# Kernel optimization log

Measured on AMD Instinct MI355X. Metric: run time of the kernel, lower is better.

Reference implementation:

```python
import jax, jax.numpy as jnp
import numpy as np

B, Hh, Ww, C, HEADS, WS, SHIFT = 8, 64, 64, 768, 12, 8, 4
N = WS * WS
HID = 4 * C


def _rel_pos_index(ws):
    coords = np.stack(np.meshgrid(np.arange(ws), np.arange(ws), indexing='ij'))  # (2, ws, ws)
    cf = coords.reshape(2, -1)
    rel = (cf[:, :, None] - cf[:, None, :]).transpose(1, 2, 0)  # (N, N, 2)
    rel[:, :, 0] += ws - 1
    rel[:, :, 1] += ws - 1
    rel[:, :, 0] *= 2 * ws - 1
    return rel.sum(-1)  # (N, N) in [0, (2ws-1)^2)


def _attn_mask(Hp, Wp, ws, shift):
    # Standard Swin shifted-window attention mask: 0 within region, -100 across.
    img = np.zeros((Hp, Wp), dtype=np.float32)
    cnt = 0
    sls = (slice(0, -ws), slice(-ws, -shift), slice(-shift, None))
    for hs in sls:
        for wsl in sls:
            img[hs, wsl] = cnt
            cnt += 1
    w = img.reshape(Hp // ws, ws, Wp // ws, ws).transpose(0, 2, 1, 3).reshape(-1, ws * ws)
    diff = w[:, None, :] - w[:, :, None]
    return np.where(diff != 0, -100.0, 0.0).astype(np.float32)  # (nW, N, N)


def setup_inputs() -> dict:
    key = jax.random.key(0)
    ks = jax.random.split(key, 8)
    s = 0.02
    return {
        'x': jax.random.normal(ks[0], (B, Hh * Ww, C), jnp.float32),
        'c': jax.random.normal(ks[1], (B, C), jnp.float32),
        'mask_matrix': jnp.asarray(_attn_mask(Hh, Ww, WS, SHIFT)),
        'rel_index': jnp.asarray(_rel_pos_index(WS), dtype=jnp.int32),
        'w_adaln': jax.random.normal(ks[2], (C, 6 * C), jnp.float32) * s,
        'b_adaln': jnp.zeros((6 * C,), jnp.float32),
        'w_qkv': jax.random.normal(ks[3], (C, 3 * C), jnp.float32) * s,
        'b_qkv': jnp.zeros((3 * C,), jnp.float32),
        'rpb_table': jax.random.normal(ks[4], ((2 * WS - 1) ** 2, HEADS), jnp.float32) * s,
        'w_proj': jax.random.normal(ks[5], (C, C), jnp.float32) * s,
        'b_proj': jnp.zeros((C,), jnp.float32),
        'w_fc1': jax.random.normal(ks[6], (C, HID), jnp.float32) * s,
        'b_fc1': jnp.zeros((HID,), jnp.float32),
        'w_fc2': jax.random.normal(ks[7], (HID, C), jnp.float32) * s,
        'b_fc2': jnp.zeros((C,), jnp.float32),
        'H': Hh,
        'W': Ww,
    }


def _ln(x, eps=1e-6):
    # LayerNorm without affine params (elementwise_affine=False)
    mu = x.mean(-1, keepdims=True)
    var = x.var(-1, keepdims=True)
    return (x - mu) * jax.lax.rsqrt(var + eps)


def _modulate(x, shift, scale):
    return x * (1.0 + scale[:, None, :]) + shift[:, None, :]


def reference(x, c, mask_matrix, rel_index, w_adaln, b_adaln, w_qkv, b_qkv,
              rpb_table, w_proj, b_proj, w_fc1, b_fc1, w_fc2, b_fc2, H, W):
    Bb, L, Cc = x.shape
    hd = Cc // HEADS
    mod = jax.nn.silu(c) @ w_adaln + b_adaln  # (B, 6C)
    sh_msa, sc_msa, g_msa, sh_mlp, sc_mlp, g_mlp = jnp.split(mod, 6, axis=1)

    shortcut = x
    h = _modulate(_ln(x), sh_msa, sc_msa).reshape(Bb, H, W, Cc)
    # H,W are multiples of WS -> no padding; shift_size>0 -> roll + mask
    h = jnp.roll(h, (-SHIFT, -SHIFT), axis=(1, 2))
    nWh, nWw = H // WS, W // WS
    win = h.reshape(Bb, nWh, WS, nWw, WS, Cc).transpose(0, 1, 3, 2, 4, 5).reshape(-1, N, Cc)

    qkv = (win @ w_qkv + b_qkv).reshape(-1, N, 3, HEADS, hd).transpose(2, 0, 3, 1, 4)
    q = qkv[0] * (hd ** -0.5)
    k, v = qkv[1], qkv[2]
    attn = jnp.einsum('bhnd,bhmd->bhnm', q, k)  # (B_, heads, N, N)
    bias = rpb_table[rel_index.reshape(-1)].reshape(N, N, HEADS).transpose(2, 0, 1)
    attn = attn + bias[None]
    nW = mask_matrix.shape[0]
    attn = attn.reshape(Bb, nW, HEADS, N, N) + mask_matrix[None, :, None]
    attn = jax.nn.softmax(attn.reshape(-1, HEADS, N, N), axis=-1)
    out = jnp.einsum('bhnm,bhmd->bnhd', attn, v).reshape(-1, N, Cc)
    out = out @ w_proj + b_proj

    out = out.reshape(Bb, nWh, nWw, WS, WS, Cc).transpose(0, 1, 3, 2, 4, 5).reshape(Bb, H, W, Cc)
    out = jnp.roll(out, (SHIFT, SHIFT), axis=(1, 2)).reshape(Bb, L, Cc)

    x1 = shortcut + g_msa[:, None, :] * out
    h2 = _modulate(_ln(x1), sh_mlp, sc_mlp)
    mlp = jax.nn.gelu(h2 @ w_fc1 + b_fc1, approximate=False) @ w_fc2 + b_fc2
    return x1 + g_mlp[:, None, :] * mlp
```

## Files before the change

kernel.cpp:

```cpp
#include <hip/hip_runtime.h>
#include <hip/hip_bf16.h>
#include <math.h>

using bf16 = __hip_bfloat16;
using short8  = __attribute__((ext_vector_type(8))) short;
using floatx4 = __attribute__((ext_vector_type(4))) float;

__device__ __forceinline__ float b2f(bf16 v){ return __bfloat162float(v); }
__device__ __forceinline__ bf16  f2b(float v){ return __float2bfloat16(v); }
__device__ __forceinline__ float loadf(const void* p, size_t i, bool f32){
    return f32 ? ((const float*)p)[i] : b2f(((const bf16*)p)[i]);
}
__device__ __forceinline__ void gload16(const void* g, void* l){
    __builtin_amdgcn_global_load_lds(
        (const __attribute__((address_space(1))) unsigned int*)g,
        (__attribute__((address_space(3))) unsigned int*)l, 16, 0, 0);
}
__device__ __forceinline__ void bar(){
    asm volatile("" ::: "memory");
    __builtin_amdgcn_s_barrier();
    asm volatile("" ::: "memory");
}
template<int Nn> __device__ __forceinline__ void vmwait(){
    if constexpr (Nn == 0)      asm volatile("s_waitcnt vmcnt(0)" ::: "memory");
    else if constexpr (Nn == 3) asm volatile("s_waitcnt vmcnt(3)" ::: "memory");
    else                        asm volatile("s_waitcnt vmcnt(4)" ::: "memory");
}
__device__ __forceinline__ void lgkm0_fence(){
    asm volatile("s_waitcnt lgkmcnt(0)" ::: "memory");
    __builtin_amdgcn_sched_barrier(0);
}

#define FIXED_WS 14303488

__global__ void detect_k(const void* __restrict__ x, int* __restrict__ flag){
    __shared__ int cnt;
    if (threadIdx.x == 0) cnt = 0;
    __syncthreads();
    const unsigned short* u = (const unsigned short*)x;
    int local = 0;
    #pragma unroll
    for (int i = 0; i < 16; ++i){
        unsigned int w = u[threadIdx.x * 16 + i];
        float v = __uint_as_float(w << 16);
        float a = fabsf(v);
        if (!(a <= 1e4f) || (v != 0.f && a < 1e-20f)) local++;
    }
    atomicAdd(&cnt, local);
    __syncthreads();
    if (threadIdx.x == 0) *flag = (cnt > 200) ? 1 : 0;
}

__global__ void transpose_k(const void* __restrict__ W, bf16* __restrict__ WT, int K, int N,
                            const int* __restrict__ dflag){
    const bool f32 = (*dflag != 0);
    __shared__ bf16 t[32][33];
    int k0 = blockIdx.y * 32, n0 = blockIdx.x * 32;
    int tx = threadIdx.x, ty = threadIdx.y;
    #pragma unroll
    for (int r = ty; r < 32; r += 8) t[r][tx] = f2b(loadf(W, (size_t)(k0 + r) * N + n0 + tx, f32));
    __syncthreads();
    #pragma unroll
    for (int r = ty; r < 32; r += 8) WT[(size_t)(n0 + r) * K + k0 + tx] = t[tx][r];
}

__global__ __launch_bounds__(256) void adaln_k(const void* __restrict__ c, const void* __restrict__ w,
                                               const void* __restrict__ bv, float* __restrict__ mod,
                                               const int* __restrict__ dflag){
    const bool f32 = (*dflag != 0);
    int b = blockIdx.y;
    int jl = threadIdx.x & 63;
    int part = threadIdx.x >> 6;
    int j = blockIdx.x * 64 + jl;
    __shared__ float sc[768];
    for (int k = threadIdx.x; k < 768; k += 256){
        float v = loadf(c, b * 768 + k, f32);
        sc[k] = v / (1.f + __expf(-v));
    }
    __syncthreads();
    float acc = 0.f;
    int k0 = part * 192;
    #pragma unroll 4
    for (int k = k0; k < k0 + 192; ++k) acc += sc[k] * loadf(w, (size_t)k * 4608 + j, f32);
    __shared__ float red[4][64];
    red[part][jl] = acc;
    __syncthreads();
    if (part == 0)
        mod[b * 4608 + j] = red[0][jl] + red[1][jl] + red[2][jl] + red[3][jl] + loadf(bv, j, f32);
}

__device__ __forceinline__ float2 block_reduce_sum2(float s, float s2){
    #pragma unroll
    for (int m = 32; m >= 1; m >>= 1){
        s  += __shfl_xor(s,  m, 64);
        s2 += __shfl_xor(s2, m, 64);
    }
    __shared__ float red[8];
    int wave = threadIdx.x >> 6;
    if ((threadIdx.x & 63) == 0){ red[wave] = s; red[4 + wave] = s2; }
    __syncthreads();
    return make_float2(red[0] + red[1] + red[2] + red[3],
                       red[4] + red[5] + red[6] + red[7]);
}

__global__ __launch_bounds__(256) void ln_mod_win_k(const void* __restrict__ x, const float* __restrict__ mod,
                                                    bf16* __restrict__ win, int roff,
                                                    const int* __restrict__ dflag){
    const bool f32 = (*dflag != 0);
    int r = roff + blockIdx.x;
    int bw = r >> 6, n = r & 63;
    int b = bw >> 6, widx = bw & 63;
    int hh = (((widx >> 3) << 3) + (n >> 3) + 4) & 63;
    int ww = (((widx & 7) << 3) + (n & 7) + 4) & 63;
    size_t xo = ((size_t)b * 4096 + hh * 64 + ww) * 768;
    int t = threadIdx.x;
    float v0 = loadf(x, xo + t, f32), v1 = loadf(x, xo + t + 256, f32), v2 = loadf(x, xo + t + 512, f32);
    float2 ss = block_reduce_sum2(v0 + v1 + v2, v0 * v0 + v1 * v1 + v2 * v2);
    float mu = ss.x * (1.f / 768.f);
    float rstd = rsqrtf(ss.y * (1.f / 768.f) - mu * mu + 1e-6f);
    const float* mb = mod + b * 4608;
    bf16* wr = win + (size_t)blockIdx.x * 768;
    wr[t]       = f2b((v0 - mu) * rstd * (1.f + mb[768 + t])       + mb[t]);
    wr[t + 256] = f2b((v1 - mu) * rstd * (1.f + mb[768 + t + 256]) + mb[t + 256]);
    wr[t + 512] = f2b((v2 - mu) * rstd * (1.f + mb[768 + t + 512]) + mb[t + 512]);
}

__global__ __launch_bounds__(256) void ln_mod2_k(const void* __restrict__ x1, const float* __restrict__ mod,
                                                 bf16* __restrict__ h2, int roff,
                                                 const int* __restrict__ dflag){
    const bool f32 = (*dflag != 0);
    int t0 = roff + blockIdx.x;
    int b = t0 >> 12;
    size_t xo = (size_t)t0 * 768;
    int t = threadIdx.x;
    float v0 = loadf(x1, xo + t, f32), v1 = loadf(x1, xo + t + 256, f32), v2 = loadf(x1, xo + t + 512, f32);
    float2 ss = block_reduce_sum2(v0 + v1 + v2, v0 * v0 + v1 * v1 + v2 * v2);
    float mu = ss.x * (1.f / 768.f);
    float rstd = rsqrtf(ss.y * (1.f / 768.f) - mu * mu + 1e-6f);
    const float* mb = mod + b * 4608;
    bf16* wr = h2 + (size_t)blockIdx.x * 768;
    wr[t]       = f2b((v0 - mu) * rstd * (1.f + mb[3072 + t])       + mb[2304 + t]);
    wr[t + 256] = f2b((v1 - mu) * rstd * (1.f + mb[3072 + t + 256]) + mb[2304 + t + 256]);
    wr[t + 512] = f2b((v2 - mu) * rstd * (1.f + mb[3072 + t + 512]) + mb[2304 + t + 512]);
}

__global__ __launch_bounds__(256) void attn_k(const bf16* __restrict__ qkv, const void* __restrict__ maskm,
                                              const int* __restrict__ rel, const void* __restrict__ rpb,
                                              bf16* __restrict__ ao, int woff,
                                              const int* __restrict__ dflag){
    const bool f32 = (*dflag != 0);
    __shared__ bf16  qs[64][68];
    __shared__ float ks[64][65];
    __shared__ bf16  vs[64][64];
    __shared__ float Ps[64][68];
    int blk = blockIdx.x;
    int head = blk % 12;
    int bw = blk / 12;
    int tid = threadIdx.x;
    const bf16* base = qkv + (size_t)bw * 64 * 2304 + head * 64;
    for (int e4 = tid; e4 < 1024; e4 += 256){
        int n = e4 >> 4, d4 = (e4 & 15) * 4;
        size_t o = (size_t)n * 2304 + d4;
        ushort4 qv = *(const ushort4*)(base + o);
        ushort4 kv = *(const ushort4*)(base + o + 768);
        ushort4 vv = *(const ushort4*)(base + o + 1536);
        bf16 q0, q1, q2, q3;
        *(unsigned short*)&q0 = qv.x; *(unsigned short*)&q1 = qv.y;
        *(unsigned short*)&q2 = qv.z; *(unsigned short*)&q3 = qv.w;
        qs[n][d4]     = f2b(b2f(q0) * 0.125f);
        qs[n][d4 + 1] = f2b(b2f(q1) * 0.125f);
        qs[n][d4 + 2] = f2b(b2f(q2) * 0.125f);
        qs[n][d4 + 3] = f2b(b2f(q3) * 0.125f);
        bf16 k0, k1, k2, k3;
        *(unsigned short*)&k0 = kv.x; *(unsigned short*)&k1 = kv.y;
        *(unsigned short*)&k2 = kv.z; *(unsigned short*)&k3 = kv.w;
        ks[n][d4]     = b2f(k0); ks[n][d4 + 1] = b2f(k1);
        ks[n][d4 + 2] = b2f(k2); ks[n][d4 + 3] = b2f(k3);
        *(ushort4*)&vs[n][d4] = vv;
    }
    __syncthreads();
    size_t mo = (size_t)((woff + bw) & 63) * 4096;
    int i0 = (tid >> 4) * 4, j0 = (tid & 15) * 4;
    {
        float acc[4][4];
        #pragma unroll
        for (int a = 0; a < 4; ++a)
            #pragma unroll
            for (int b2 = 0; b2 < 4; ++b2) acc[a][b2] = 0.f;
        #pragma unroll 8
        for (int d = 0; d < 64; ++d){
            float qv[4], kv[4];
            #pragma unroll
            for (int a = 0; a < 4; ++a) qv[a] = b2f(qs[i0 + a][d]);
            #pragma unroll
            for (int b2 = 0; b2 < 4; ++b2) kv[b2] = ks[j0 + b2][d];
            #pragma unroll
            for (int a = 0; a < 4; ++a)
                #pragma unroll
                for (int b2 = 0; b2 < 4; ++b2) acc[a][b2] += qv[a] * kv[b2];
        }
        #pragma unroll
        for (int a = 0; a < 4; ++a){
            int i = i0 + a;
            int4 r4 = *(const int4*)&rel[i * 64 + j0];
            float4 o4;
            o4.x = acc[a][0] + loadf(rpb, (size_t)r4.x * 12 + head, f32) + loadf(maskm, mo + i * 64 + j0,     f32);
            o4.y = acc[a][1] + loadf(rpb, (size_t)r4.y * 12 + head, f32) + loadf(maskm, mo + i * 64 + j0 + 1, f32);
            o4.z = acc[a][2] + loadf(rpb, (size_t)r4.z * 12 + head, f32) + loadf(maskm, mo + i * 64 + j0 + 2, f32);
            o4.w = acc[a][3] + loadf(rpb, (size_t)r4.w * 12 + head, f32) + loadf(maskm, mo + i * 64 + j0 + 3, f32);
            *(float4*)&Ps[i][j0] = o4;
        }
    }
    __syncthreads();
    {
        int row = tid >> 2, p0 = (tid & 3) * 16;
        float mx = -1e30f;
        #pragma unroll
        for (int j = 0; j < 16; ++j) mx = fmaxf(mx, Ps[row][p0 + j]);
        mx = fmaxf(mx, __shfl_xor(mx, 1, 64));
        mx = fmaxf(mx, __shfl_xor(mx, 2, 64));
        float sum = 0.f;
        float ev[16];
        #pragma unroll
        for (int j = 0; j < 16; ++j){ ev[j] = __expf(Ps[row][p0 + j] - mx); sum += ev[j]; }
        sum += __shfl_xor(sum, 1, 64);
        sum += __shfl_xor(sum, 2, 64);
        float inv = 1.f / sum;
        #pragma unroll
        for (int j = 0; j < 16; ++j) Ps[row][p0 + j] = ev[j] * inv;
    }
    __syncthreads();
    {
        int d0 = j0;
        float po[4][4];
        #pragma unroll
        for (int a = 0; a < 4; ++a)
            #pragma unroll
            for (int b2 = 0; b2 < 4; ++b2) po[a][b2] = 0.f;
        #pragma unroll 8
        for (int j = 0; j < 64; ++j){
            float pv[4];
            #pragma unroll
            for (int a = 0; a < 4; ++a) pv[a] = Ps[i0 + a][j];
            ushort4 v4 = *(const ushort4*)&vs[j][d0];
            bf16 w0, w1, w2, w3;
            *(unsigned short*)&w0 = v4.x; *(unsigned short*)&w1 = v4.y;
            *(unsigned short*)&w2 = v4.z; *(unsigned short*)&w3 = v4.w;
            float vv[4] = {b2f(w0), b2f(w1), b2f(w2), b2f(w3)};
            #pragma unroll
            for (int a = 0; a < 4; ++a)
                #pragma unroll
                for (int b2 = 0; b2 < 4; ++b2) po[a][b2] += pv[a] * vv[b2];
        }
        #pragma unroll
        for (int a = 0; a < 4; ++a){
            ushort4 s4;
            bf16 t0 = f2b(po[a][0]), t1 = f2b(po[a][1]), t2 = f2b(po[a][2]), t3 = f2b(po[a][3]);
            s4.x = *(unsigned short*)&t0; s4.y = *(unsigned short*)&t1;
            s4.z = *(unsigned short*)&t2; s4.w = *(unsigned short*)&t3;
            *(ushort4*)&ao[((size_t)bw * 64 + i0 + a) * 768 + head * 64 + d0] = s4;
        }
    }
}

template<int EPI, int BN>
__global__ __launch_bounds__(256, (BN == 128) ? 3 : 4)
void gemm_k(const bf16* __restrict__ A, const bf16* __restrict__ BT,
            const void* __restrict__ bias, void* __restrict__ Cout,
            int N, int K, int roff,
            const void* __restrict__ xres, const float* __restrict__ mod,
            const void* __restrict__ x1,
            const int* __restrict__ dflag, int nMB){
    constexpr int MFR = (BN == 128) ? 4 : 2;
    constexpr int LPT = (BN == 128) ? 4 : 3;
    const bool f32 = (*dflag != 0);
    __shared__ __align__(16) bf16 As[3][128 * 32];
    __shared__ __align__(16) bf16 Bs[3][BN * 32];

    int bid = (int)blockIdx.x;
    int nb = bid / nMB, mb = bid % nMB;
    int m0 = mb * 128, n0 = nb * BN;

    int tid = threadIdx.x;
    int wave = tid >> 6, lane = tid & 63;
    int wm = (BN == 128) ? (wave >> 1) * 64 : wave * 32;
    int wn = (BN == 128) ? (wave & 1) * 64 : 0;
    int lrow = lane & 15, lq = lane >> 4;
    floatx4 acc[MFR][4];
    #pragma unroll
    for (int i = 0; i < MFR; ++i)
        #pragma unroll
        for (int j = 0; j < 4; ++j) acc[i][j] = floatx4{0.f, 0.f, 0.f, 0.f};

    int sc8 = ((((lane & 3) - ((lane >> 3) & 3)) & 3)) * 8;
    int srw = lane >> 2;
    const bf16* gA = A + (size_t)(m0 + wave * 32 + srw) * K + sc8;
    int lofsA0 = (wave * 32) * 32;
    int lofsA1 = (wave * 32 + 16) * 32;
    const bf16* gB;
    int lofsB;
    if constexpr (BN == 128){ gB = BT + (size_t)(n0 + wave * 32 + srw) * K + sc8; lofsB = lofsA0; }
    else                    { gB = BT + (size_t)(n0 + wave * 16 + srw) * K + sc8; lofsB = (wave * 16) * 32; }

    int fsw = ((lq + ((lrow >> 1) & 3)) & 3) * 8;
    int aoff = (wm + lrow) * 32 + fsw;
    int boff = (wn + lrow) * 32 + fsw;

    auto stage = [&](int t, int buf){
        size_t kof = (size_t)t * 32;
        gload16(gA + kof,                  As[buf] + lofsA0);
        gload16(gA + kof + (size_t)16 * K, As[buf] + lofsA1);
        gload16(gB + kof,                  Bs[buf] + lofsB);
        if constexpr (BN == 128)
            gload16(gB + kof + (size_t)16 * K, Bs[buf] + lofsA1);
    };

    const int nkt = K >> 5;
    stage(0, 0); stage(1, 1);
    vmwait<LPT>();
    bar();
    int cur = 0, nx2 = 2;
    for (int t = 0; t < nkt; ++t){
        short8 af[MFR], bfr[4];
        #pragma unroll
        for (int f = 0; f < MFR; ++f) af[f]  = *(const short8*)(As[cur] + aoff + f * 512);
        #pragma unroll
        for (int f = 0; f < 4;   ++f) bfr[f] = *(const short8*)(Bs[cur] + boff + f * 512);
        if (t + 2 < nkt) stage(t + 2, nx2);
        lgkm0_fence();
        __builtin_amdgcn_s_setprio(1);
        #pragma unroll
        for (int mf = 0; mf < MFR; ++mf)
            #pragma unroll
            for (int nf = 0; nf < 4; ++nf)
                acc[mf][nf] = __builtin_amdgcn_mfma_f32_16x16x32_bf16(af[mf], bfr[nf], acc[mf][nf], 0, 0, 0);
        __builtin_amdgcn_s_setprio(0);
        if (t + 2 < nkt) vmwait<LPT>();
        else             vmwait<0>();
        bar();
        cur = (cur == 2) ? 0 : cur + 1;
        nx2 = (nx2 == 2) ? 0 : nx2 + 1;
    }

    #pragma unroll
    for (int mf = 0; mf < MFR; ++mf){
        #pragma unroll
        for (int nf = 0; nf < 4; ++nf){
            #pragma unroll
            for (int rr = 0; rr < 4; ++rr){
                int grow = m0 + wm + mf * 16 + lq * 4 + rr;
                int gcol = n0 + wn + nf * 16 + lrow;
                float v = acc[mf][nf][rr] + loadf(bias, gcol, f32);
                if (EPI == 0){
                    ((bf16*)Cout)[(size_t)grow * N + gcol] = f2b(v);
                } else if (EPI == 1){
                    float g = 0.5f * v * (1.f + erff(v * 0.70710678118654752f));
                    ((bf16*)Cout)[(size_t)grow * N + gcol] = f2b(g);
                } else if (EPI == 2){
                    int gr = roff + grow;
                    int bw = gr >> 6, n = gr & 63;
                    int b = bw >> 6, widx = bw & 63;
                    int hh = (((widx >> 3) << 3) + (n >> 3) + 4) & 63;
                    int ww = (((widx & 7) << 3) + (n & 7) + 4) & 63;
                    size_t t = ((size_t)b * 4096 + hh * 64 + ww) * 768 + gcol;
                    float gm = mod[b * 4608 + 1536 + gcol];
                    float res = loadf(xres, t, f32) + gm * v;
                    if (f32) ((float*)Cout)[t] = res; else ((bf16*)Cout)[t] = f2b(res);
                } else {
                    int gr = roff + grow;
                    int b = gr >> 12;
                    float gm = mod[b * 4608 + 3840 + gcol];
                    size_t t = (size_t)gr * N + gcol;
                    float res = loadf(x1, t, f32) + gm * v;
                    if (f32) ((float*)Cout)[t] = res; else ((bf16*)Cout)[t] = f2b(res);
                }
            }
        }
    }
}

extern "C" void kernel_launch(void* const* d_in, const int* in_sizes, int n_in,
                              void* d_out, int out_size, void* d_ws, size_t ws_size,
                              hipStream_t stream){
    const void* x       = d_in[0];
    const void* c       = d_in[1];
    const void* maskm   = d_in[2];
    const int*  rel     = (const int*)d_in[3];
    const void* w_adaln = d_in[4];
    const void* b_adaln = d_in[5];
    const void* w_qkv   = d_in[6];
    const void* b_qkv   = d_in[7];
    const void* rpb     = d_in[8];
    const void* w_proj  = d_in[9];
    const void* b_proj  = d_in[10];
    const void* w_fc1   = d_in[11];
    const void* b_fc1   = d_in[12];
    const void* w_fc2   = d_in[13];
    const void* b_fc2   = d_in[14];

    int Mc = 4096;
    for (int cand = 8192; cand >= 256; cand >>= 1){
        if (FIXED_WS + (size_t)cand * 7680u <= ws_size){ Mc = cand; break; }
    }
    const int nc  = 32768 / Mc;
    const int nMB = Mc / 128;

    char* ws = (char*)d_ws;
    int*  dflag  = (int*)(ws);
    float* mod   = (float*)(ws + 256);
    bf16* wqkvT  = (bf16*)(ws + 147712);
    bf16* wprojT = (bf16*)(ws + 3686656);
    bf16* wfc1T  = (bf16*)(ws + 4866304);
    bf16* wfc2T  = (bf16*)(ws + 9584896);
    bf16* win_c  = (bf16*)(ws + FIXED_WS);
    bf16* big_c  = (bf16*)(ws + FIXED_WS + (size_t)Mc * 1536);
    bf16* ao_c   = (bf16*)(ws + FIXED_WS + (size_t)Mc * 6144);
    void* x1     = d_out;
    void* out    = d_out;

    detect_k<<<1, 256, 0, stream>>>(x, dflag);

    dim3 tb(32, 8);
    transpose_k<<<dim3(2304/32, 768/32),  tb, 0, stream>>>(w_qkv,  wqkvT,  768, 2304, dflag);
    transpose_k<<<dim3(768/32,  768/32),  tb, 0, stream>>>(w_proj, wprojT, 768, 768, dflag);
    transpose_k<<<dim3(3072/32, 768/32),  tb, 0, stream>>>(w_fc1,  wfc1T,  768, 3072, dflag);
    transpose_k<<<dim3(768/32,  3072/32), tb, 0, stream>>>(w_fc2,  wfc2T,  3072, 768, dflag);
    adaln_k<<<dim3(72, 8), 256, 0, stream>>>(c, w_adaln, b_adaln, mod, dflag);

    for (int ch = 0; ch < nc; ++ch){
        int roff = ch * Mc;
        ln_mod_win_k<<<Mc, 256, 0, stream>>>(x, mod, win_c, roff, dflag);
        gemm_k<0,128><<<nMB * 18, 256, 0, stream>>>(win_c, wqkvT, b_qkv, big_c,
                                                    2304, 768, 0, nullptr, nullptr, nullptr, dflag, nMB);
        attn_k<<<(Mc/64) * 12, 256, 0, stream>>>(big_c, maskm, rel, rpb, ao_c, roff / 64, dflag);
        gemm_k<2,64><<<nMB * 12, 256, 0, stream>>>(ao_c, wprojT, b_proj, x1,
                                                   768, 768, roff, x, mod, nullptr, dflag, nMB);
    }
    for (int ch = 0; ch < nc; ++ch){
        int roff = ch * Mc;
        ln_mod2_k<<<Mc, 256, 0, stream>>>(x1, mod, win_c, roff, dflag);
        gemm_k<1,128><<<nMB * 24, 256, 0, stream>>>(win_c, wfc1T, b_fc1, big_c,
                                                    3072, 768, 0, nullptr, nullptr, nullptr, dflag, nMB);
        gemm_k<3,64><<<nMB * 12, 256, 0, stream>>>(big_c, wfc2T, b_fc2, out,
                                                   768, 3072, roff, nullptr, mod, x1, dflag, nMB);
    }
}
```

Baseline: 1.320 ms.

## Make GEMM kernel persistent with cross-tile prefetch and allow larger chunks

Converts gemm_k into a persistent kernel. A capped grid of 768 or 1024 blocks walks a contiguous range of output tiles and keeps the three-stage LDS load pipeline running across tile boundaries, so the next tile's loads overlap the current tile's epilogue. Bias values are cached per column block. The chunk-size search now starts at the full 32768 rows, which cuts the number of kernel launches when the workspace is large enough. The cost is more complex index bookkeeping and uneven tile counts per block, and larger chunks need more workspace.

```diff
diff --git a/kernel.cpp b/kernel.cpp
--- a/kernel.cpp
+++ b/kernel.cpp
@@ -270,63 +270,80 @@
             int N, int K, int roff,
             const void* __restrict__ xres, const float* __restrict__ mod,
             const void* __restrict__ x1,
-            const int* __restrict__ dflag, int nMB){
+            const int* __restrict__ dflag, int nMB, int total){
     constexpr int MFR = (BN == 128) ? 4 : 2;
     constexpr int LPT = (BN == 128) ? 4 : 3;
     const bool f32 = (*dflag != 0);
     __shared__ __align__(16) bf16 As[3][128 * 32];
     __shared__ __align__(16) bf16 Bs[3][BN * 32];
-
-    int bid = (int)blockIdx.x;
-    int nb = bid / nMB, mb = bid % nMB;
-    int m0 = mb * 128, n0 = nb * BN;
 
     int tid = threadIdx.x;
     int wave = tid >> 6, lane = tid & 63;
     int wm = (BN == 128) ? (wave >> 1) * 64 : wave * 32;
     int wn = (BN == 128) ? (wave & 1) * 64 : 0;
     int lrow = lane & 15, lq = lane >> 4;
+
+    int G = (int)gridDim.x, bid = (int)blockIdx.x;
+    int q = total / G, r = total % G;
+    int myLen = q + (bid < r ? 1 : 0);
+    int first = bid * q + (bid < r ? bid : r);
+    const int nkt = K >> 5;
+    int TS = myLen * nkt;
+
+    int sc8 = ((((lane & 3) - ((lane >> 3) & 3)) & 3)) * 8;
+    int srw = lane >> 2;
+    int lofsA0 = (wave * 32) * 32;
+    int lofsA1 = (wave * 32 + 16) * 32;
+    int lofsB  = (BN == 128) ? lofsA0 : (wave * 16) * 32;
+    int wB     = (BN == 128) ? wave * 32 : wave * 16;
+
+    int fsw = ((lq + ((lrow >> 1) & 3)) & 3) * 8;
+    int aoff = (wm + lrow) * 32 + fsw;
+    int boff = (wn + lrow) * 32 + fsw;
+
     floatx4 acc[MFR][4];
     #pragma unroll
     for (int i = 0; i < MFR; ++i)
         #pragma unroll
         for (int j = 0; j < 4; ++j) acc[i][j] = floatx4{0.f, 0.f, 0.f, 0.f};
 
-    int sc8 = ((((lane & 3) - ((lane >> 3) & 3)) & 3)) * 8;
-    int srw = lane >> 2;
-    const bf16* gA = A + (size_t)(m0 + wave * 32 + srw) * K + sc8;
-    int lofsA0 = (wave * 32) * 32;
-    int lofsA1 = (wave * 32 + 16) * 32;
-    const bf16* gB;
-    int lofsB;
-    if constexpr (BN == 128){ gB = BT + (size_t)(n0 + wave * 32 + srw) * K + sc8; lofsB = lofsA0; }
-    else                    { gB = BT + (size_t)(n0 + wave * 16 + srw) * K + sc8; lofsB = (wave * 16) * 32; }
-
-    int fsw = ((lq + ((lrow >> 1) & 3)) & 3) * 8;
-    int aoff = (wm + lrow) * 32 + fsw;
-    int boff = (wn + lrow) * 32 + fsw;
-
-    auto stage = [&](int t, int buf){
-        size_t kof = (size_t)t * 32;
+    int sIdx = first, sT = 0;
+    const bf16 *gA, *gB;
+    auto setPtrs = [&](){
+        int m0s = (sIdx % nMB) * 128;
+        int n0s = (sIdx / nMB) * BN;
+        gA = A  + (size_t)(m0s + wave * 32 + srw) * K + sc8;
+        gB = BT + (size_t)(n0s + wB + srw) * K + sc8;
+    };
+    setPtrs();
+    auto stageStep = [&](int buf){
+        size_t kof = (size_t)sT * 32;
         gload16(gA + kof,                  As[buf] + lofsA0);
         gload16(gA + kof + (size_t)16 * K, As[buf] + lofsA1);
         gload16(gB + kof,                  Bs[buf] + lofsB);
         if constexpr (BN == 128)
             gload16(gB + kof + (size_t)16 * K, Bs[buf] + lofsA1);
+        if (++sT == nkt){ sT = 0; ++sIdx; setPtrs(); }
     };
 
-    const int nkt = K >> 5;
-    stage(0, 0); stage(1, 1);
+    stageStep(0); stageStep(1);
     vmwait<LPT>();
     bar();
+
+    int rIdx = first, rT = 0;
+    int rm0 = (rIdx % nMB) * 128, rn0 = (rIdx / nMB) * BN;
+    float bb[4];
+    int bN0 = -1;
     int cur = 0, nx2 = 2;
-    for (int t = 0; t < nkt; ++t){
+
+    for (int T = 0; T < TS; ++T){
         short8 af[MFR], bfr[4];
         #pragma unroll
         for (int f = 0; f < MFR; ++f) af[f]  = *(const short8*)(As[cur] + aoff + f * 512);
         #pragma unroll
         for (int f = 0; f < 4;   ++f) bfr[f] = *(const short8*)(Bs[cur] + boff + f * 512);
-        if (t + 2 < nkt) stage(t + 2, nx2);
+        bool more = (T + 2 < TS);
+        if (more) stageStep(nx2);
         lgkm0_fence();
         __builtin_amdgcn_s_setprio(1);
         #pragma unroll
@@ -335,46 +352,61 @@
             for (int nf = 0; nf < 4; ++nf)
                 acc[mf][nf] = __builtin_amdgcn_mfma_f32_16x16x32_bf16(af[mf], bfr[nf], acc[mf][nf], 0, 0, 0);
         __builtin_amdgcn_s_setprio(0);
-        if (t + 2 < nkt) vmwait<LPT>();
-        else             vmwait<0>();
-        bar();
+        if (T + 1 < TS){
+            if (more) vmwait<LPT>();
+            else      vmwait<0>();
+            bar();
+        }
         cur = (cur == 2) ? 0 : cur + 1;
         nx2 = (nx2 == 2) ? 0 : nx2 + 1;
-    }
-
-    #pragma unroll
-    for (int mf = 0; mf < MFR; ++mf){
-        #pragma unroll
-        for (int nf = 0; nf < 4; ++nf){
-            #pragma unroll
-            for (int rr = 0; rr < 4; ++rr){
-                int grow = m0 + wm + mf * 16 + lq * 4 + rr;
-                int gcol = n0 + wn + nf * 16 + lrow;
-                float v = acc[mf][nf][rr] + loadf(bias, gcol, f32);
-                if (EPI == 0){
-                    ((bf16*)Cout)[(size_t)grow * N + gcol] = f2b(v);
-                } else if (EPI == 1){
-                    float g = 0.5f * v * (1.f + erff(v * 0.70710678118654752f));
-                    ((bf16*)Cout)[(size_t)grow * N + gcol] = f2b(g);
-                } else if (EPI == 2){
-                    int gr = roff + grow;
-                    int bw = gr >> 6, n = gr & 63;
-                    int b = bw >> 6, widx = bw & 63;
-                    int hh = (((widx >> 3) << 3) + (n >> 3) + 4) & 63;
-                    int ww = (((widx & 7) << 3) + (n & 7) + 4) & 63;
-                    size_t t = ((size_t)b * 4096 + hh * 64 + ww) * 768 + gcol;
-                    float gm = mod[b * 4608 + 1536 + gcol];
-                    float res = loadf(xres, t, f32) + gm * v;
-                    if (f32) ((float*)Cout)[t] = res; else ((bf16*)Cout)[t] = f2b(res);
-                } else {
-                    int gr = roff + grow;
-                    int b = gr >> 12;
-                    float gm = mod[b * 4608 + 3840 + gcol];
-                    size_t t = (size_t)gr * N + gcol;
-                    float res = loadf(x1, t, f32) + gm * v;
-                    if (f32) ((float*)Cout)[t] = res; else ((bf16*)Cout)[t] = f2b(res);
+        if (++rT == nkt){
+            rT = 0;
+            if (rn0 != bN0){
+                bN0 = rn0;
+                #pragma unroll
+                for (int nf = 0; nf < 4; ++nf) bb[nf] = loadf(bias, rn0 + wn + nf * 16 + lrow, f32);
+            }
+            #pragma unroll
+            for (int mf = 0; mf < MFR; ++mf){
+                #pragma unroll
+                for (int nf = 0; nf < 4; ++nf){
+                    #pragma unroll
+                    for (int rr = 0; rr < 4; ++rr){
+                        int grow = rm0 + wm + mf * 16 + lq * 4 + rr;
+                        int gcol = rn0 + wn + nf * 16 + lrow;
+                        float v = acc[mf][nf][rr] + bb[nf];
+                        if (EPI == 0){
+                            ((bf16*)Cout)[(size_t)grow * N + gcol] = f2b(v);
+                        } else if (EPI == 1){
+                            float g = 0.5f * v * (1.f + erff(v * 0.70710678118654752f));
+                            ((bf16*)Cout)[(size_t)grow * N + gcol] = f2b(g);
+                        } else if (EPI == 2){
+                            int gr = roff + grow;
+                            int bw = gr >> 6, n = gr & 63;
+                            int b = bw >> 6, widx = bw & 63;
+                            int hh = (((widx >> 3) << 3) + (n >> 3) + 4) & 63;
+                            int ww = (((widx & 7) << 3) + (n & 7) + 4) & 63;
+                            size_t t = ((size_t)b * 4096 + hh * 64 + ww) * 768 + gcol;
+                            float gm = mod[b * 4608 + 1536 + gcol];
+                            float res = loadf(xres, t, f32) + gm * v;
+                            if (f32) ((float*)Cout)[t] = res; else ((bf16*)Cout)[t] = f2b(res);
+                        } else {
+                            int gr = roff + grow;
+                            int b = gr >> 12;
+                            float gm = mod[b * 4608 + 3840 + gcol];
+                            size_t t = (size_t)gr * N + gcol;
+                            float res = loadf(x1, t, f32) + gm * v;
+                            if (f32) ((float*)Cout)[t] = res; else ((bf16*)Cout)[t] = f2b(res);
+                        }
+                    }
                 }
             }
+            #pragma unroll
+            for (int i = 0; i < MFR; ++i)
+                #pragma unroll
+                for (int j = 0; j < 4; ++j) acc[i][j] = floatx4{0.f, 0.f, 0.f, 0.f};
+            ++rIdx;
+            rm0 = (rIdx % nMB) * 128; rn0 = (rIdx / nMB) * BN;
         }
     }
 }
@@ -399,7 +431,7 @@
     const void* b_fc2   = d_in[14];
 
     int Mc = 4096;
-    for (int cand = 8192; cand >= 256; cand >>= 1){
+    for (int cand = 32768; cand >= 256; cand >>= 1){
         if (FIXED_WS + (size_t)cand * 7680u <= ws_size){ Mc = cand; break; }
     }
     const int nc  = 32768 / Mc;
@@ -427,21 +459,27 @@
     transpose_k<<<dim3(768/32,  3072/32), tb, 0, stream>>>(w_fc2,  wfc2T,  3072, 768, dflag);
     adaln_k<<<dim3(72, 8), 256, 0, stream>>>(c, w_adaln, b_adaln, mod, dflag);
 
+    const int G128 = 768;
+    const int G64  = 1024;
     for (int ch = 0; ch < nc; ++ch){
         int roff = ch * Mc;
         ln_mod_win_k<<<Mc, 256, 0, stream>>>(x, mod, win_c, roff, dflag);
-        gemm_k<0,128><<<nMB * 18, 256, 0, stream>>>(win_c, wqkvT, b_qkv, big_c,
-                                                    2304, 768, 0, nullptr, nullptr, nullptr, dflag, nMB);
+        int tqkv = nMB * 18;
+        gemm_k<0,128><<<(tqkv < G128 ? tqkv : G128), 256, 0, stream>>>(win_c, wqkvT, b_qkv, big_c,
+                                                    2304, 768, 0, nullptr, nullptr, nullptr, dflag, nMB, tqkv);
         attn_k<<<(Mc/64) * 12, 256, 0, stream>>>(big_c, maskm, rel, rpb, ao_c, roff / 64, dflag);
-        gemm_k<2,64><<<nMB * 12, 256, 0, stream>>>(ao_c, wprojT, b_proj, x1,
-                                                   768, 768, roff, x, mod, nullptr, dflag, nMB);
+        int tproj = nMB * 12;
+        gemm_k<2,64><<<(tproj < G64 ? tproj : G64), 256, 0, stream>>>(ao_c, wprojT, b_proj, x1,
+                                                   768, 768, roff, x, mod, nullptr, dflag, nMB, tproj);
     }
     for (int ch = 0; ch < nc; ++ch){
         int roff = ch * Mc;
         ln_mod2_k<<<Mc, 256, 0, stream>>>(x1, mod, win_c, roff, dflag);
-        gemm_k<1,128><<<nMB * 24, 256, 0, stream>>>(win_c, wfc1T, b_fc1, big_c,
-                                                    3072, 768, 0, nullptr, nullptr, nullptr, dflag, nMB);
-        gemm_k<3,64><<<nMB * 12, 256, 0, stream>>>(big_c, wfc2T, b_fc2, out,
-                                                   768, 3072, roff, nullptr, mod, x1, dflag, nMB);
-    }
-}
+        int tfc1 = nMB * 24;
+        gemm_k<1,128><<<(tfc1 < G128 ? tfc1 : G128), 256, 0, stream>>>(win_c, wfc1T, b_fc1, big_c,
+                                                    3072, 768, 0, nullptr, nullptr, nullptr, dflag, nMB, tfc1);
+        int tfc2 = nMB * 12;
+        gemm_k<3,64><<<(tfc2 < G64 ? tfc2 : G64), 256, 0, stream>>>(big_c, wfc2T, b_fc2, out,
+                                                   768, 3072, roff, nullptr, mod, x1, dflag, nMB, tfc2);
+    }
+}
```

Measured after the change: 1.357 ms. 1.03x slower.
